# Kernel optimization log

Hardware: AMD Instinct MI355X
Metric: run time of the kernel (lower is better)

Reference implementation:

```python
import jax, jax.numpy as jnp
import numpy as np

N_HEADS = 32
N_KV = 8
HEAD_DIM = 64
DIM = 2048
B, T = 4, 1024


def apply_rope(x, cos, sin):
    # x: [B, H, T, D]; cos/sin: [T, D//2]
    Tlen = x.shape[2]
    c = cos[:Tlen][None, None]  # [1,1,T,D/2]
    s = sin[:Tlen][None, None]
    x_even = x[..., 0::2]
    x_odd = x[..., 1::2]
    r_even = x_even * c - x_odd * s
    r_odd = x_even * s + x_odd * c
    # interleave back: out[...,0::2]=r_even, out[...,1::2]=r_odd
    return jnp.stack([r_even, r_odd], axis=-1).reshape(x.shape)


def setup_inputs() -> dict:
    key = jax.random.key(0)
    ks = jax.random.split(key, 7)
    sc = 0.02
    return {
        "x": jax.random.normal(ks[0], (B, T, DIM), jnp.float32),
        "cos": jax.random.normal(ks[1], (T, HEAD_DIM // 2), jnp.float32),
        "sin": jax.random.normal(ks[2], (T, HEAD_DIM // 2), jnp.float32),
        "Wq": jax.random.normal(ks[3], (N_HEADS * HEAD_DIM, DIM), jnp.float32) * sc,
        "Wk": jax.random.normal(ks[4], (N_KV * HEAD_DIM, DIM), jnp.float32) * sc,
        "Wv": jax.random.normal(ks[5], (N_KV * HEAD_DIM, DIM), jnp.float32) * sc,
        "Wo": jax.random.normal(ks[6], (DIM, N_HEADS * HEAD_DIM), jnp.float32) * sc,
    }


def reference(x, cos, sin, Wq, Wk, Wv, Wo):
    Bb, Tt, _ = x.shape
    rep = N_HEADS // N_KV
    # projections (torch Linear: y = x @ W.T)
    q = (x @ Wq.T).reshape(Bb, Tt, N_HEADS, HEAD_DIM).transpose(0, 2, 1, 3)
    k = (x @ Wk.T).reshape(Bb, Tt, N_KV, HEAD_DIM).transpose(0, 2, 1, 3)
    v = (x @ Wv.T).reshape(Bb, Tt, N_KV, HEAD_DIM).transpose(0, 2, 1, 3)
    q = apply_rope(q, cos, sin)
    k = apply_rope(k, cos, sin)
    k = jnp.repeat(k, rep, axis=1)  # [B, n_heads, T, D]
    v = jnp.repeat(v, rep, axis=1)
    scale = HEAD_DIM ** (-0.5)
    scores = jnp.einsum('bhqd,bhkd->bhqk', q, k) * scale
    causal = jnp.triu(jnp.ones((Tt, Tt), dtype=bool), k=1)
    scores = jnp.where(causal[None, None], -jnp.inf, scores)
    attn = jax.nn.softmax(scores, axis=-1)
    out = jnp.einsum('bhqk,bhkd->bhqd', attn, v)
    out = out.transpose(0, 2, 1, 3).reshape(Bb, Tt, N_HEADS * HEAD_DIM)
    return out @ Wo.T
```

## Files before the change

### kernel.cpp

```cpp
#include <hip/hip_runtime.h>
#include <math.h>

#define GAS __attribute__((address_space(1)))
#define LAS __attribute__((address_space(3)))

typedef __attribute__((ext_vector_type(4))) float f32x4;
typedef __attribute__((ext_vector_type(8))) short bf16x8;
typedef __attribute__((ext_vector_type(4))) short bf16x4;

#define MFMA(a,b,c)   __builtin_amdgcn_mfma_f32_16x16x32_bf16((a),(b),(c),0,0,0)
#define MFMA16(a,b,c) __builtin_amdgcn_mfma_f32_16x16x16bf16_1k((a),(b),(c),0,0,0)

#if __has_builtin(__builtin_amdgcn_exp2f)
#define EXP2(x) __builtin_amdgcn_exp2f(x)
#else
#define EXP2(x) exp2f(x)
#endif

__device__ __forceinline__ void gl_lds16(const void* g, void* l) {
    __builtin_amdgcn_global_load_lds((const GAS unsigned*)g, (LAS unsigned*)l, 16, 0, 0);
}

__device__ __forceinline__ short f2bf(float f) {
    union { float f; unsigned u; } v; v.f = f;
    unsigned r = (v.u + 0x7fff + ((v.u >> 16) & 1)) >> 16;
    return (short)r;
}

__device__ __forceinline__ void castN(const float* __restrict__ s, short* __restrict__ d,
                                      int n4, int gid, int gsz) {
    for (int i = gid; i < n4; i += gsz) {
        float4 v = ((const float4*)s)[i];
        short4 o = make_short4(f2bf(v.x), f2bf(v.y), f2bf(v.z), f2bf(v.w));
        ((short4*)d)[i] = o;
    }
}

__global__ __launch_bounds__(256)
void cast_all(const float* __restrict__ x,  const float* __restrict__ wq,
              const float* __restrict__ wk, const float* __restrict__ wv,
              const float* __restrict__ wo,
              short* __restrict__ xb, short* __restrict__ wqkv, short* __restrict__ wob) {
    int gid = blockIdx.x*256 + threadIdx.x;
    int gsz = gridDim.x*256;
    castN(x,  xb,               (4096*2048)/4, gid, gsz);
    castN(wq, wqkv,             (2048*2048)/4, gid, gsz);
    castN(wk, wqkv + 2048*2048, (512*2048)/4,  gid, gsz);
    castN(wv, wqkv + 2560*2048, (512*2048)/4,  gid, gsz);
    castN(wo, wob,              (2048*2048)/4, gid, gsz);
}

template<int MODE>
__global__ __launch_bounds__(512, 6)
void gemm_mfma(const short* __restrict__ A, const short* __restrict__ Bw,
               int M, int N, int K, float* __restrict__ Cf,
               short* __restrict__ qo, short* __restrict__ ko, short* __restrict__ vo,
               const float* __restrict__ cosb, const float* __restrict__ sinb)
{
    __shared__ short smem[24576];

    const int tid  = threadIdx.x;
    const int lane = tid & 63, wvi = tid >> 6;
    const int l15  = lane & 15, quad = lane >> 4;
    const int wm   = wvi >> 2,  wn   = wvi & 3;
    const int m0   = blockIdx.y * 128, n0 = blockIdx.x * 128;

    const int srow   = lane >> 2;
    const int schunk = ((lane & 3) ^ ((lane >> 3) & 3)) << 3;
    const short* gA = A  + (size_t)(m0 + wvi*16 + srow)*K + schunk;
    const short* gB = Bw + (size_t)(n0 + wvi*16 + srow)*K + schunk;

    const int swz     = (quad ^ ((l15 >> 1) & 3)) << 3;
    const int ardbase = (wm*64 + l15)*32 + swz;
    const int brdbase = 4096 + (wn*32 + l15)*32 + swz;

    f32x4 acc[4][2] = {};

#define SBAR  __builtin_amdgcn_s_barrier()
#define PRIO1 __builtin_amdgcn_s_setprio(1)
#define PRIO0 __builtin_amdgcn_s_setprio(0)
#define VMW(n) asm volatile("s_waitcnt vmcnt(" #n ")" ::: "memory")

#define STG(h, s) do { const int _k = (h)<<5;                                      \
    gl_lds16(gA + _k,  &smem[(s)*8192 + wvi*512]);                                 \
    gl_lds16(gB + _k,  &smem[(s)*8192 + 4096 + wvi*512]);                          \
} while(0)

    const int H = K >> 5;

    STG(0, 0); STG(1, 1);
    VMW(2); SBAR;

    int sc = 0;
    for (int h = 0; h < H; ++h) {
        bf16x8 a[4], b[2];
        const int sb = sc*8192;
        #pragma unroll
        for (int i = 0; i < 4; i++) a[i] = *(const bf16x8*)&smem[sb + ardbase + i*512];
        #pragma unroll
        for (int j = 0; j < 2; j++) b[j] = *(const bf16x8*)&smem[sb + brdbase + j*512];

        if (h + 2 < H) {
            int s2 = sc + 2; if (s2 >= 3) s2 -= 3;
            STG(h + 2, s2);
        }

        PRIO1;
        #pragma unroll
        for (int i = 0; i < 4; i++)
            #pragma unroll
            for (int j = 0; j < 2; j++) acc[i][j] = MFMA(a[i], b[j], acc[i][j]);
        PRIO0;

        if (h + 2 < H)      { VMW(2); }
        else if (h + 1 < H) { VMW(0); }
        SBAR;
        sc = (sc == 2) ? 0 : sc + 1;
    }
#undef STG
#undef VMW

    if (MODE == 0) {
        #pragma unroll
        for (int i = 0; i < 4; i++)
            #pragma unroll
            for (int j = 0; j < 2; j++) {
                int n  = n0 + wn*32 + j*16 + l15;
                int mb = m0 + wm*64 + i*16 + quad*4;
                #pragma unroll
                for (int r = 0; r < 4; r++)
                    Cf[(size_t)(mb + r)*N + n] = acc[i][j][r];
            }
    } else {
        #pragma unroll
        for (int i = 0; i < 4; i++)
            #pragma unroll
            for (int j = 0; j < 2; j++) {
                int n  = n0 + wn*32 + j*16 + l15;
                int mb = m0 + wm*64 + i*16 + quad*4;
                if (n >= 2560) {
                    int bq = mb >> 10, t0 = mb & 1023;
                    int hv = (n - 2560) >> 6, d = (n - 2560) & 63;
                    short4 s4 = make_short4(f2bf(acc[i][j][0]), f2bf(acc[i][j][1]),
                                            f2bf(acc[i][j][2]), f2bf(acc[i][j][3]));
                    *(short4*)&vo[(((size_t)(bq*8 + hv)*64 + d) << 10) + t0] = s4;
                } else {
                    #pragma unroll
                    for (int r = 0; r < 4; r++) {
                        int m = mb + r;
                        int b = m >> 10, t = m & 1023;
                        float val = acc[i][j][r];
                        float part = __shfl_xor(val, 1);
                        int d2 = (n & 63) >> 1;
                        float c = cosb[t*32 + d2], s = sinb[t*32 + d2];
                        val = (n & 1) ? (part*s + val*c) : (val*c - part*s);
                        if (n < 2048) {
                            val *= 0.18033688f;
                            qo[(((size_t)(b*32 + (n>>6))*1024 + t) << 6) + (n & 63)] = f2bf(val);
                        } else {
                            ko[(((size_t)(b*8 + ((n-2048)>>6))*1024 + t) << 6) + ((n-2048) & 63)] = f2bf(val);
                        }
                    }
                }
            }
    }
}

__global__ __launch_bounds__(1024, 8)
void attn_mfma(const short* __restrict__ q_ws, const short* __restrict__ k_ws,
               const short* __restrict__ vt_ws, short* __restrict__ o_ws)
{
    __shared__ short Ks[2][4096];
    __shared__ short Vs[2][4608];

    const int tid = threadIdx.x, lane = tid & 63, wv = tid >> 6;
    const int qt = (blockIdx.z & 2) ? blockIdx.x : (15 - blockIdx.x);
    const int kvh = blockIdx.y, b = blockIdx.z;
    const int hq = wv & 3, rgrp = wv >> 2;
    const int head = kvh*4 + hq;
    const size_t qbase  = ((size_t)(b*32 + head)) << 16;
    const size_t kvbase = ((size_t)(b*8  + kvh )) << 16;
    const short* kt = k_ws  + kvbase;
    const short* vt = vt_ws + kvbase;
    const int l15 = lane & 15, quad = lane >> 4;

    const bool vstager = (tid < 512);
    const int vrow = tid >> 3, vcol = (tid & 7)*8;
    const int g = tid & 511;
    const int kc = g >> 8, kr = (g >> 2) & 63, dq = (g & 3)*8;

    if (vstager) {
        bf16x8 v0 = *(const bf16x8*)(vt + (size_t)vrow*1024 + vcol);
        *(bf16x8*)&Vs[0][vrow*72 + vcol] = v0;
    } else {
        gl_lds16(kt + (size_t)kr*64 + kc*32 + dq, &Ks[0][(wv - 8)*512]);
    }

    const short* qp = q_ws + qbase + (size_t)(qt*64 + rgrp*16 + l15)*64 + quad*8;
    bf16x8 aq0 = *(const bf16x8*)qp;
    bf16x8 aq1 = *(const bf16x8*)(qp + 32);

    f32x4 o_acc[4] = {};
    float lsum = 0.f;
    const int qrel = rgrp*16 + l15;

    for (int c = 0; c <= qt; c++) {
        const int cb = c & 1, nb = cb ^ 1;
        __syncthreads();
        bf16x8 vreg;
        const bool pre = (c < qt);
        if (pre) {
            if (vstager)
                vreg = *(const bf16x8*)(vt + (size_t)vrow*1024 + (c+1)*64 + vcol);
            else
                gl_lds16(kt + (size_t)((c+1)*64 + kr)*64 + kc*32 + dq,
                         &Ks[nb][(wv - 8)*512]);
        }

        f32x4 s_acc[4];
        #pragma unroll
        for (int nt = 0; nt < 4; nt++) {
            bf16x8 kf0 = *(const bf16x8*)&Ks[cb][(nt*16 + l15)*32 + quad*8];
            bf16x8 kf1 = *(const bf16x8*)&Ks[cb][2048 + (nt*16 + l15)*32 + quad*8];
            f32x4 z = {};
            z = MFMA(kf0, aq0, z);
            s_acc[nt] = MFMA(kf1, aq1, z);
        }

        bf16x4 pb[4];
        if (c == qt) {
            #pragma unroll
            for (int nt = 0; nt < 4; nt++)
                #pragma unroll
                for (int r = 0; r < 4; r++) {
                    float p = (nt*16 + quad*4 + r > qrel) ? 0.f : EXP2(s_acc[nt][r]);
                    lsum += p;
                    pb[nt][r] = f2bf(p);
                }
        } else {
            #pragma unroll
            for (int nt = 0; nt < 4; nt++)
                #pragma unroll
                for (int r = 0; r < 4; r++) {
                    float p = EXP2(s_acc[nt][r]);
                    lsum += p;
                    pb[nt][r] = f2bf(p);
                }
        }

        if (pre && vstager)
            *(bf16x8*)&Vs[nb][vrow*72 + vcol] = vreg;

        #pragma unroll
        for (int dt = 0; dt < 4; dt++)
            #pragma unroll
            for (int nt = 0; nt < 4; nt++) {
                bf16x4 vf = *(const bf16x4*)&Vs[cb][(dt*16 + l15)*72 + nt*16 + quad*4];
                o_acc[dt] = MFMA16(vf, pb[nt], o_acc[dt]);
            }
    }

    lsum += __shfl_xor(lsum, 16);
    lsum += __shfl_xor(lsum, 32);
    float inv = 1.f / lsum;
    short* orow = o_ws + ((size_t)(b*1024 + qt*64 + qrel))*2048 + head*64;
    #pragma unroll
    for (int dt = 0; dt < 4; dt++) {
        short4 s4 = make_short4(f2bf(o_acc[dt][0]*inv), f2bf(o_acc[dt][1]*inv),
                                f2bf(o_acc[dt][2]*inv), f2bf(o_acc[dt][3]*inv));
        *(short4*)&orow[dt*16 + quad*4] = s4;
    }
}

extern "C" void kernel_launch(void* const* d_in, const int* in_sizes, int n_in,
                              void* d_out, int out_size, void* d_ws, size_t ws_size,
                              hipStream_t stream) {
    const float* x    = (const float*)d_in[0];
    const float* cosb = (const float*)d_in[1];
    const float* sinb = (const float*)d_in[2];
    const float* Wq   = (const float*)d_in[3];
    const float* Wk   = (const float*)d_in[4];
    const float* Wv   = (const float*)d_in[5];
    const float* Wo   = (const float*)d_in[6];
    float* out = (float*)d_out;

    short* xb   = (short*)d_ws;
    short* wqkv = xb   + 8388608;
    short* wob  = wqkv + 6291456;
    short* q_ws = wob  + 4194304;
    short* k_ws = q_ws + 8388608;
    short* v_ws = k_ws + 2097152;
    short* o_ws = v_ws + 2097152;

    cast_all<<<2048, 256, 0, stream>>>(x, Wq, Wk, Wv, Wo, xb, wqkv, wob);
    gemm_mfma<1><<<dim3(24, 32), 512, 0, stream>>>(xb, wqkv, 4096, 3072, 2048,
                                                   nullptr, q_ws, k_ws, v_ws, cosb, sinb);
    attn_mfma<<<dim3(16, 8, 4), 1024, 0, stream>>>(q_ws, k_ws, v_ws, o_ws);
    gemm_mfma<0><<<dim3(16, 32), 512, 0, stream>>>(o_ws, wob, 4096, 2048, 2048,
                                                   out, nullptr, nullptr, nullptr, nullptr, nullptr);
}
```

Before: 262.7 us.

## Pair complementary causal query tiles per block and swizzle V LDS layout

Each attention block now handles two query tiles (qt and 15-qt), so the K/V chunks staged into LDS are reused by both tiles and every block does the same amount of causal work. The grid is halved to 256 blocks. The padded V shared layout (stride 72) is replaced with an XOR-swizzled stride-64 layout to avoid bank conflicts without padding. This raises register pressure (two accumulator sets), so the launch-bounds occupancy hint drops to 4, and fewer blocks may leave some compute units underused.

```diff
diff --git a/kernel.cpp b/kernel.cpp
--- a/kernel.cpp
+++ b/kernel.cpp
@@ -166,15 +166,16 @@
     }
 }
 
-__global__ __launch_bounds__(1024, 8)
+__global__ __launch_bounds__(1024, 4)
 void attn_mfma(const short* __restrict__ q_ws, const short* __restrict__ k_ws,
                const short* __restrict__ vt_ws, short* __restrict__ o_ws)
 {
     __shared__ short Ks[2][4096];
-    __shared__ short Vs[2][4608];
+    __shared__ short Vs[2][4096];
 
     const int tid = threadIdx.x, lane = tid & 63, wv = tid >> 6;
-    const int qt = (blockIdx.z & 2) ? blockIdx.x : (15 - blockIdx.x);
+    const int qtA = blockIdx.x;
+    const int qtB = 15 - blockIdx.x;
     const int kvh = blockIdx.y, b = blockIdx.z;
     const int hq = wv & 3, rgrp = wv >> 2;
     const int head = kvh*4 + hq;
@@ -185,90 +186,110 @@
     const int l15 = lane & 15, quad = lane >> 4;
 
     const bool vstager = (tid < 512);
-    const int vrow = tid >> 3, vcol = (tid & 7)*8;
+    const int vrow = tid >> 3, vchunk = tid & 7;
+    const int vdst = vrow*64 + ((vchunk ^ (vrow & 7)) << 3);
     const int g = tid & 511;
     const int kc = g >> 8, kr = (g >> 2) & 63, dq = (g & 3)*8;
 
     if (vstager) {
-        bf16x8 v0 = *(const bf16x8*)(vt + (size_t)vrow*1024 + vcol);
-        *(bf16x8*)&Vs[0][vrow*72 + vcol] = v0;
+        bf16x8 v0 = *(const bf16x8*)(vt + (size_t)vrow*1024 + vchunk*8);
+        *(bf16x8*)&Vs[0][vdst] = v0;
     } else {
         gl_lds16(kt + (size_t)kr*64 + kc*32 + dq, &Ks[0][(wv - 8)*512]);
     }
 
-    const short* qp = q_ws + qbase + (size_t)(qt*64 + rgrp*16 + l15)*64 + quad*8;
-    bf16x8 aq0 = *(const bf16x8*)qp;
-    bf16x8 aq1 = *(const bf16x8*)(qp + 32);
-
-    f32x4 o_acc[4] = {};
-    float lsum = 0.f;
+    const short* qpA = q_ws + qbase + (size_t)(qtA*64 + rgrp*16 + l15)*64 + quad*8;
+    const short* qpB = q_ws + qbase + (size_t)(qtB*64 + rgrp*16 + l15)*64 + quad*8;
+    bf16x8 aqA0 = *(const bf16x8*)qpA, aqA1 = *(const bf16x8*)(qpA + 32);
+    bf16x8 aqB0 = *(const bf16x8*)qpB, aqB1 = *(const bf16x8*)(qpB + 32);
+
+    f32x4 oA[4] = {}, oB[4] = {};
+    float lsA = 0.f, lsB = 0.f;
     const int qrel = rgrp*16 + l15;
 
-    for (int c = 0; c <= qt; c++) {
+    for (int c = 0; c <= qtB; c++) {
         const int cb = c & 1, nb = cb ^ 1;
         __syncthreads();
         bf16x8 vreg;
-        const bool pre = (c < qt);
+        const bool pre = (c < qtB);
         if (pre) {
             if (vstager)
-                vreg = *(const bf16x8*)(vt + (size_t)vrow*1024 + (c+1)*64 + vcol);
+                vreg = *(const bf16x8*)(vt + (size_t)vrow*1024 + (c+1)*64 + vchunk*8);
             else
                 gl_lds16(kt + (size_t)((c+1)*64 + kr)*64 + kc*32 + dq,
                          &Ks[nb][(wv - 8)*512]);
         }
-
-        f32x4 s_acc[4];
+        const bool actA = (c <= qtA);
+
+        bf16x8 kf0[4], kf1[4];
         #pragma unroll
         for (int nt = 0; nt < 4; nt++) {
-            bf16x8 kf0 = *(const bf16x8*)&Ks[cb][(nt*16 + l15)*32 + quad*8];
-            bf16x8 kf1 = *(const bf16x8*)&Ks[cb][2048 + (nt*16 + l15)*32 + quad*8];
+            kf0[nt] = *(const bf16x8*)&Ks[cb][(nt*16 + l15)*32 + quad*8];
+            kf1[nt] = *(const bf16x8*)&Ks[cb][2048 + (nt*16 + l15)*32 + quad*8];
+        }
+
+        bf16x4 pbB[4];
+        #pragma unroll
+        for (int nt = 0; nt < 4; nt++) {
             f32x4 z = {};
-            z = MFMA(kf0, aq0, z);
-            s_acc[nt] = MFMA(kf1, aq1, z);
-        }
-
-        bf16x4 pb[4];
-        if (c == qt) {
-            #pragma unroll
-            for (int nt = 0; nt < 4; nt++)
+            z = MFMA(kf0[nt], aqB0, z);
+            f32x4 s = MFMA(kf1[nt], aqB1, z);
+            #pragma unroll
+            for (int r = 0; r < 4; r++) {
+                float p;
+                if (c == qtB) p = (nt*16 + quad*4 + r > qrel) ? 0.f : EXP2(s[r]);
+                else          p = EXP2(s[r]);
+                lsB += p;
+                pbB[nt][r] = f2bf(p);
+            }
+        }
+
+        bf16x4 pbA[4];
+        if (actA) {
+            #pragma unroll
+            for (int nt = 0; nt < 4; nt++) {
+                f32x4 z = {};
+                z = MFMA(kf0[nt], aqA0, z);
+                f32x4 s = MFMA(kf1[nt], aqA1, z);
                 #pragma unroll
                 for (int r = 0; r < 4; r++) {
-                    float p = (nt*16 + quad*4 + r > qrel) ? 0.f : EXP2(s_acc[nt][r]);
-                    lsum += p;
-                    pb[nt][r] = f2bf(p);
+                    float p;
+                    if (c == qtA) p = (nt*16 + quad*4 + r > qrel) ? 0.f : EXP2(s[r]);
+                    else          p = EXP2(s[r]);
+                    lsA += p;
+                    pbA[nt][r] = f2bf(p);
                 }
-        } else {
-            #pragma unroll
-            for (int nt = 0; nt < 4; nt++)
-                #pragma unroll
-                for (int r = 0; r < 4; r++) {
-                    float p = EXP2(s_acc[nt][r]);
-                    lsum += p;
-                    pb[nt][r] = f2bf(p);
-                }
+            }
         }
 
         if (pre && vstager)
-            *(bf16x8*)&Vs[nb][vrow*72 + vcol] = vreg;
+            *(bf16x8*)&Vs[nb][vdst] = vreg;
 
         #pragma unroll
         for (int dt = 0; dt < 4; dt++)
             #pragma unroll
             for (int nt = 0; nt < 4; nt++) {
-                bf16x4 vf = *(const bf16x4*)&Vs[cb][(dt*16 + l15)*72 + nt*16 + quad*4];
-                o_acc[dt] = MFMA16(vf, pb[nt], o_acc[dt]);
-            }
-    }
-
-    lsum += __shfl_xor(lsum, 16);
-    lsum += __shfl_xor(lsum, 32);
-    float inv = 1.f / lsum;
-    short* orow = o_ws + ((size_t)(b*1024 + qt*64 + qrel))*2048 + head*64;
+                const int ck = nt*2 + (quad >> 1);
+                bf16x4 vf = *(const bf16x4*)&Vs[cb][(dt*16 + l15)*64 +
+                                ((ck ^ (l15 & 7)) << 3) + (quad & 1)*4];
+                oB[dt] = MFMA16(vf, pbB[nt], oB[dt]);
+                if (actA) oA[dt] = MFMA16(vf, pbA[nt], oA[dt]);
+            }
+    }
+
+    lsA += __shfl_xor(lsA, 16); lsA += __shfl_xor(lsA, 32);
+    lsB += __shfl_xor(lsB, 16); lsB += __shfl_xor(lsB, 32);
+    float invA = 1.f / lsA, invB = 1.f / lsB;
+    short* orowA = o_ws + ((size_t)(b*1024 + qtA*64 + qrel))*2048 + head*64;
+    short* orowB = o_ws + ((size_t)(b*1024 + qtB*64 + qrel))*2048 + head*64;
     #pragma unroll
     for (int dt = 0; dt < 4; dt++) {
-        short4 s4 = make_short4(f2bf(o_acc[dt][0]*inv), f2bf(o_acc[dt][1]*inv),
-                                f2bf(o_acc[dt][2]*inv), f2bf(o_acc[dt][3]*inv));
-        *(short4*)&orow[dt*16 + quad*4] = s4;
+        short4 sA = make_short4(f2bf(oA[dt][0]*invA), f2bf(oA[dt][1]*invA),
+                                f2bf(oA[dt][2]*invA), f2bf(oA[dt][3]*invA));
+        *(short4*)&orowA[dt*16 + quad*4] = sA;
+        short4 sB = make_short4(f2bf(oB[dt][0]*invB), f2bf(oB[dt][1]*invB),
+                                f2bf(oB[dt][2]*invB), f2bf(oB[dt][3]*invB));
+        *(short4*)&orowB[dt*16 + quad*4] = sB;
     }
 }
 
@@ -295,7 +316,7 @@
     cast_all<<<2048, 256, 0, stream>>>(x, Wq, Wk, Wv, Wo, xb, wqkv, wob);
     gemm_mfma<1><<<dim3(24, 32), 512, 0, stream>>>(xb, wqkv, 4096, 3072, 2048,
                                                    nullptr, q_ws, k_ws, v_ws, cosb, sinb);
-    attn_mfma<<<dim3(16, 8, 4), 1024, 0, stream>>>(q_ws, k_ws, v_ws, o_ws);
+    attn_mfma<<<dim3(8, 8, 4), 1024, 0, stream>>>(q_ws, k_ws, v_ws, o_ws);
     gemm_mfma<0><<<dim3(16, 32), 512, 0, stream>>>(o_ws, wob, 4096, 2048, 2048,
                                                    out, nullptr, nullptr, nullptr, nullptr, nullptr);
 }
```

Measured after the change: 271.0 us. +3.1%, slower.

## Process 128-key chunks per attention iteration with XOR-swizzled V tile

Applied to the files above, without the earlier changes.

Doubles the KV chunk size in the attention loop from 64 to 128 keys. This halves the number of loop iterations and __syncthreads barriers per query tile and issues more MFMAs between syncs. The V tile in LDS switches from a padded row layout to an XOR swizzle to avoid bank conflicts. LDS use per block roughly doubles, and the causal diagonal chunk now computes up to 64 fully masked keys for even query tiles.

```diff
diff --git a/kernel.cpp b/kernel.cpp
--- a/kernel.cpp
+++ b/kernel.cpp
@@ -170,8 +170,8 @@
 void attn_mfma(const short* __restrict__ q_ws, const short* __restrict__ k_ws,
                const short* __restrict__ vt_ws, short* __restrict__ o_ws)
 {
-    __shared__ short Ks[2][4096];
-    __shared__ short Vs[2][4608];
+    __shared__ short Ks[2][8192];
+    __shared__ short Vs[2][8192];
 
     const int tid = threadIdx.x, lane = tid & 63, wv = tid >> 6;
     const int qt = (blockIdx.z & 2) ? blockIdx.x : (15 - blockIdx.x);
@@ -185,15 +185,20 @@
     const int l15 = lane & 15, quad = lane >> 4;
 
     const bool vstager = (tid < 512);
-    const int vrow = tid >> 3, vcol = (tid & 7)*8;
-    const int g = tid & 511;
-    const int kc = g >> 8, kr = (g >> 2) & 63, dq = (g & 3)*8;
+    const int vrow = tid >> 3, vch = tid & 7;
+    const int vdst0 = vrow*128 + (((vch    ) ^ (vrow & 15)) << 3);
+    const int vdst1 = vrow*128 + (((vch + 8) ^ (vrow & 15)) << 3);
+    const int g  = tid & 511;
+    const int kr = (g >> 2) & 127, dq = (g & 3)*8;
 
     if (vstager) {
-        bf16x8 v0 = *(const bf16x8*)(vt + (size_t)vrow*1024 + vcol);
-        *(bf16x8*)&Vs[0][vrow*72 + vcol] = v0;
+        bf16x8 v0 = *(const bf16x8*)(vt + (size_t)vrow*1024 + vch*8);
+        bf16x8 v1 = *(const bf16x8*)(vt + (size_t)vrow*1024 + 64 + vch*8);
+        *(bf16x8*)&Vs[0][vdst0] = v0;
+        *(bf16x8*)&Vs[0][vdst1] = v1;
     } else {
-        gl_lds16(kt + (size_t)kr*64 + kc*32 + dq, &Ks[0][(wv - 8)*512]);
+        gl_lds16(kt + (size_t)kr*64 +      dq, &Ks[0][(wv - 8)*512]);
+        gl_lds16(kt + (size_t)kr*64 + 32 + dq, &Ks[0][4096 + (wv - 8)*512]);
     }
 
     const short* qp = q_ws + qbase + (size_t)(qt*64 + rgrp*16 + l15)*64 + quad*8;
@@ -203,59 +208,65 @@
     f32x4 o_acc[4] = {};
     float lsum = 0.f;
     const int qrel = rgrp*16 + l15;
-
-    for (int c = 0; c <= qt; c++) {
+    const int qg = qt*64 + qrel;
+    const int lastc = qt >> 1;
+
+    for (int c = 0; c <= lastc; c++) {
         const int cb = c & 1, nb = cb ^ 1;
         __syncthreads();
-        bf16x8 vreg;
-        const bool pre = (c < qt);
+        bf16x8 vr0, vr1;
+        const bool pre = (c < lastc);
         if (pre) {
-            if (vstager)
-                vreg = *(const bf16x8*)(vt + (size_t)vrow*1024 + (c+1)*64 + vcol);
-            else
-                gl_lds16(kt + (size_t)((c+1)*64 + kr)*64 + kc*32 + dq,
+            if (vstager) {
+                vr0 = *(const bf16x8*)(vt + (size_t)vrow*1024 + (c+1)*128 + vch*8);
+                vr1 = *(const bf16x8*)(vt + (size_t)vrow*1024 + (c+1)*128 + 64 + vch*8);
+            } else {
+                gl_lds16(kt + (size_t)((c+1)*128 + kr)*64 +      dq,
                          &Ks[nb][(wv - 8)*512]);
+                gl_lds16(kt + (size_t)((c+1)*128 + kr)*64 + 32 + dq,
+                         &Ks[nb][4096 + (wv - 8)*512]);
+            }
         }
 
-        f32x4 s_acc[4];
-        #pragma unroll
-        for (int nt = 0; nt < 4; nt++) {
+        bf16x4 pb[8];
+        #pragma unroll
+        for (int nt = 0; nt < 8; nt++) {
             bf16x8 kf0 = *(const bf16x8*)&Ks[cb][(nt*16 + l15)*32 + quad*8];
-            bf16x8 kf1 = *(const bf16x8*)&Ks[cb][2048 + (nt*16 + l15)*32 + quad*8];
+            bf16x8 kf1 = *(const bf16x8*)&Ks[cb][4096 + (nt*16 + l15)*32 + quad*8];
             f32x4 z = {};
             z = MFMA(kf0, aq0, z);
-            s_acc[nt] = MFMA(kf1, aq1, z);
-        }
-
-        bf16x4 pb[4];
-        if (c == qt) {
-            #pragma unroll
-            for (int nt = 0; nt < 4; nt++)
+            f32x4 s = MFMA(kf1, aq1, z);
+            if (c == lastc) {
                 #pragma unroll
                 for (int r = 0; r < 4; r++) {
-                    float p = (nt*16 + quad*4 + r > qrel) ? 0.f : EXP2(s_acc[nt][r]);
+                    int kg = c*128 + nt*16 + quad*4 + r;
+                    float p = (kg > qg) ? 0.f : EXP2(s[r]);
                     lsum += p;
                     pb[nt][r] = f2bf(p);
                 }
-        } else {
-            #pragma unroll
-            for (int nt = 0; nt < 4; nt++)
+            } else {
                 #pragma unroll
                 for (int r = 0; r < 4; r++) {
-                    float p = EXP2(s_acc[nt][r]);
+                    float p = EXP2(s[r]);
                     lsum += p;
                     pb[nt][r] = f2bf(p);
                 }
+            }
         }
 
-        if (pre && vstager)
-            *(bf16x8*)&Vs[nb][vrow*72 + vcol] = vreg;
+        if (pre && vstager) {
+            *(bf16x8*)&Vs[nb][vdst0] = vr0;
+            *(bf16x8*)&Vs[nb][vdst1] = vr1;
+        }
 
         #pragma unroll
         for (int dt = 0; dt < 4; dt++)
             #pragma unroll
-            for (int nt = 0; nt < 4; nt++) {
-                bf16x4 vf = *(const bf16x4*)&Vs[cb][(dt*16 + l15)*72 + nt*16 + quad*4];
+            for (int nt = 0; nt < 8; nt++) {
+                const int ck  = nt*2 + (quad >> 1);
+                const int row = dt*16 + l15;
+                bf16x4 vf = *(const bf16x4*)&Vs[cb][row*128 +
+                                ((ck ^ (row & 15)) << 3) + (quad & 1)*4];
                 o_acc[dt] = MFMA16(vf, pb[nt], o_acc[dt]);
             }
     }
```

Measured after the change: 317.1 us. +20.7%, slower.
